# Optimization experiments

Hardware: AMD Instinct MI355X
Metric: run time of the kernel (lower is better)

The kernel has to match this reference:

```python
import jax, jax.numpy as jnp
import numpy as np

B, N, G, H, W = 8, 2000, 100, 320, 320
TRAIN_ROIS = 200
ROI_POS_RATIO = 0.33
NUM_POS = int(TRAIN_ROIS * ROI_POS_RATIO)   # 66 positive slots
NUM_NEG = TRAIN_ROIS - NUM_POS              # 134 negative slots
MASK_H, MASK_W = 28, 28
BBOX_STD = jnp.asarray([0.1, 0.1, 0.2, 0.2], jnp.float32)
EPS = 1e-8


def _rand_boxes(key, shape):
    c = jax.random.uniform(key, shape + (2, 2), dtype=jnp.float32)
    lo, hi = c.min(axis=-2), c.max(axis=-2)
    return jnp.stack([lo[..., 0], lo[..., 1], hi[..., 0], hi[..., 1]], axis=-1)


def setup_inputs() -> dict:
    key = jax.random.key(0)
    k1, k2, k3, k4 = jax.random.split(key, 4)
    proposals = _rand_boxes(k1, (B, N))
    valid = (jnp.arange(G) < G - 20)  # emulate zero-padded GT slots
    prior_boxes = _rand_boxes(k2, (B, G)) * valid[None, :, None]
    prior_class_ids = jax.random.randint(k3, (B, G), 1, 81).astype(jnp.int32) * valid[None, :]
    prior_masks = jax.random.bernoulli(k4, 0.5, (B, H, W, G))
    return {"proposals": proposals, "prior_class_ids": prior_class_ids,
            "prior_boxes": prior_boxes, "prior_masks": prior_masks}


def _iou(a, b):
    # a [N,4], b [G,4], boxes are (y1,x1,y2,x2) -> [N,G]
    y1 = jnp.maximum(a[:, None, 0], b[None, :, 0])
    x1 = jnp.maximum(a[:, None, 1], b[None, :, 1])
    y2 = jnp.minimum(a[:, None, 2], b[None, :, 2])
    x2 = jnp.minimum(a[:, None, 3], b[None, :, 3])
    inter = jnp.maximum(y2 - y1, 0.0) * jnp.maximum(x2 - x1, 0.0)
    area_a = (a[:, 2] - a[:, 0]) * (a[:, 3] - a[:, 1])
    area_b = (b[:, 2] - b[:, 0]) * (b[:, 3] - b[:, 1])
    union = area_a[:, None] + area_b[None, :] - inter
    return inter / jnp.maximum(union, EPS)


def _box_refinement(box, gt):
    h = jnp.maximum(box[:, 2] - box[:, 0], EPS)
    w = jnp.maximum(box[:, 3] - box[:, 1], EPS)
    cy = box[:, 0] + 0.5 * h
    cx = box[:, 1] + 0.5 * w
    gh = jnp.maximum(gt[:, 2] - gt[:, 0], EPS)
    gw = jnp.maximum(gt[:, 3] - gt[:, 1], EPS)
    gcy = gt[:, 0] + 0.5 * gh
    gcx = gt[:, 1] + 0.5 * gw
    return jnp.stack([(gcy - cy) / h, (gcx - cx) / w,
                      jnp.log(gh / h), jnp.log(gw / w)], axis=-1)


def _crop_resize(mask, box):
    # bilinear crop-and-resize of one [H,W] mask to [MASK_H,MASK_W]
    Hm, Wm = mask.shape
    y1, x1, y2, x2 = box[0], box[1], box[2], box[3]
    fy = jnp.arange(MASK_H, dtype=jnp.float32) / (MASK_H - 1)
    fx = jnp.arange(MASK_W, dtype=jnp.float32) / (MASK_W - 1)
    ys = jnp.clip(y1 * (Hm - 1) + fy * (y2 - y1) * (Hm - 1), 0.0, Hm - 1.0)
    xs = jnp.clip(x1 * (Wm - 1) + fx * (x2 - x1) * (Wm - 1), 0.0, Wm - 1.0)
    y0 = jnp.clip(jnp.floor(ys).astype(jnp.int32), 0, Hm - 2)
    x0 = jnp.clip(jnp.floor(xs).astype(jnp.int32), 0, Wm - 2)
    wy, wx = ys - y0, xs - x0
    r0, r1 = mask[y0], mask[y0 + 1]            # [mh, W]
    c00, c01 = r0[:, x0], r0[:, x0 + 1]        # [mh, mw]
    c10, c11 = r1[:, x0], r1[:, x0 + 1]
    top = c00 * (1 - wx)[None, :] + c01 * wx[None, :]
    bot = c10 * (1 - wx)[None, :] + c11 * wx[None, :]
    return top * (1 - wy)[:, None] + bot * wy[:, None]


def _targets_single(proposals, class_ids, gt_boxes, gt_masks):
    valid_prop = jnp.any(jnp.abs(proposals) > 0, axis=1)   # trim zero-padded proposals
    valid_gt = jnp.any(jnp.abs(gt_boxes) > 0, axis=1)      # trim zero-padded GT
    iou = jnp.where(valid_gt[None, :] & valid_prop[:, None],
                    _iou(proposals, gt_boxes), -1.0)       # [N,G]
    roi_iou_max = iou.max(axis=1)

    # positive ROIs: IoU >= 0.5; deterministic hardest-first selection (top-k)
    pos = roi_iou_max >= 0.5
    _, pos_idx = jax.lax.top_k(jnp.where(pos, roi_iou_max, -1.0), NUM_POS)
    pos_count = jnp.minimum(pos.sum(), NUM_POS)
    pos_ok = jnp.arange(NUM_POS) < pos_count

    # negatives: IoU < 0.5, keep positive:negative ratio
    neg = (roi_iou_max < 0.5) & valid_prop
    _, neg_idx = jax.lax.top_k(jnp.where(neg, roi_iou_max, -2.0), NUM_NEG)
    neg_count = (pos_count.astype(jnp.float32) / ROI_POS_RATIO).astype(jnp.int32) - pos_count
    neg_count = jnp.minimum(jnp.minimum(neg_count, neg.sum()), NUM_NEG)
    neg_ok = jnp.arange(NUM_NEG) < neg_count

    pos_rois = jnp.where(pos_ok[:, None], proposals[pos_idx], 0.0)
    gt_assign = jnp.argmax(iou[pos_idx], axis=1)            # [NUM_POS]
    roi_gt = gt_boxes[gt_assign]
    tgt_class = jnp.where(pos_ok, class_ids[gt_assign], 0)
    deltas = jnp.where(pos_ok[:, None], _box_refinement(pos_rois, roi_gt) / BBOX_STD, 0.0)

    # gather assigned GT masks and crop-resize by the positive ROI box (use_mini_mask=False)
    masks_g = jnp.transpose(gt_masks, (2, 0, 1)).astype(jnp.float32)  # [G,H,W]
    crops = jax.vmap(_crop_resize)(masks_g[gt_assign], pos_rois)      # [NUM_POS,mh,mw]
    tgt_mask = jnp.where(pos_ok[:, None, None], jnp.round(crops), 0.0)

    neg_rois = jnp.where(neg_ok[:, None], proposals[neg_idx], 0.0)
    rois = jnp.concatenate([pos_rois, neg_rois], axis=0)
    tgt_class = jnp.concatenate([tgt_class, jnp.zeros((NUM_NEG,), tgt_class.dtype)])
    deltas = jnp.concatenate([deltas, jnp.zeros((NUM_NEG, 4), deltas.dtype)])
    tgt_mask = jnp.concatenate([tgt_mask, jnp.zeros((NUM_NEG, MASK_H, MASK_W), tgt_mask.dtype)])
    return rois, tgt_class, deltas, tgt_mask


def reference(proposals, prior_class_ids, prior_boxes, prior_masks):
    return jax.vmap(_targets_single)(proposals, prior_class_ids, prior_boxes, prior_masks)
```

## Files before the change

kernel.cpp:

```cpp
#include <hip/hip_runtime.h>

#define Bn 8
#define Nn 2000
#define Gn 100
#define Hm 320
#define Wm 320
#define NUM_POS 66
#define NUM_NEG 134
#define TRAIN_ROIS 200
#define MASK_H 28
#define MASK_W 28
#define EPSf 1e-8f

__global__ void k_iou(const float* __restrict__ proposals,
                      const float* __restrict__ gt_boxes,
                      const unsigned int* __restrict__ masks_raw,
                      float* __restrict__ ws_m, int* __restrict__ ws_g,
                      int* __restrict__ flag) {
#pragma clang fp contract(off)
    int b = blockIdx.x;
    int tid = threadIdx.x;
    __shared__ float4 sgt[Gn];
    __shared__ unsigned char svalid[Gn];
    for (int g = tid; g < Gn; g += blockDim.x) {
        const float* q = gt_boxes + (b * Gn + g) * 4;
        float4 bx = make_float4(q[0], q[1], q[2], q[3]);
        sgt[g] = bx;
        svalid[g] = (fabsf(bx.x) > 0.f) || (fabsf(bx.y) > 0.f) ||
                    (fabsf(bx.z) > 0.f) || (fabsf(bx.w) > 0.f);
    }
    if (b == 0 && tid == 0) {
        int f = 0;
        for (int i = 0; i < 64; ++i) {
            unsigned int w = masks_raw[i];
            if (w == 0x3F800000u) { f = 2; break; }
            if (w > 1u) f = 1;
        }
        *flag = f;
    }
    __syncthreads();
    for (int i = tid; i < Nn; i += blockDim.x) {
        const float* pp = proposals + (b * Nn + i) * 4;
        float p0 = pp[0], p1 = pp[1], p2 = pp[2], p3 = pp[3];
        bool vp = (fabsf(p0) > 0.f) || (fabsf(p1) > 0.f) ||
                  (fabsf(p2) > 0.f) || (fabsf(p3) > 0.f);
        float area_a = (p2 - p0) * (p3 - p1);
        float m = -1.0f;
        int best = 0;
        for (int g = 0; g < Gn; ++g) {
            float val = -1.0f;
            if (vp && svalid[g]) {
                float4 q = sgt[g];
                float y1 = fmaxf(p0, q.x);
                float x1 = fmaxf(p1, q.y);
                float y2 = fminf(p2, q.z);
                float x2 = fminf(p3, q.w);
                float inter = fmaxf(y2 - y1, 0.f) * fmaxf(x2 - x1, 0.f);
                float area_b = (q.z - q.x) * (q.w - q.y);
                float uni = area_a + area_b - inter;
                val = inter / fmaxf(uni, EPSf);
            }
            if (val > m) { m = val; best = g; }
        }
        ws_m[b * Nn + i] = m;
        ws_g[b * Nn + i] = best;
    }
}

__global__ __launch_bounds__(1024) void k_select(
        const float* __restrict__ proposals,
        const int* __restrict__ class_ids,
        const float* __restrict__ gt_boxes,
        const float* __restrict__ ws_m,
        const int* __restrict__ ws_g,
        int* __restrict__ posmap,
        float* __restrict__ out) {
#pragma clang fp contract(off)
    int b = blockIdx.x;
    int tid = threadIdx.x;
    __shared__ unsigned long long key[2048];
    __shared__ int cnt_pos, cnt_neg;
    if (tid == 0) { cnt_pos = 0; cnt_neg = 0; }
    __syncthreads();
    for (int i = tid; i < 2048; i += 1024) {
        unsigned long long k;
        if (i < Nn) {
            float m = ws_m[b * Nn + i];
            if (m >= 0.5f) atomicAdd(&cnt_pos, 1);
            else if (m >= 0.0f) atomicAdd(&cnt_neg, 1);
            unsigned int u = __float_as_uint(m);
            u = (u & 0x80000000u) ? ~u : (u | 0x80000000u);
            k = ((unsigned long long)u << 32) | (unsigned int)(~(unsigned int)i);
        } else {
            k = 0ull;
        }
        key[i] = k;
    }
    __syncthreads();
    for (int kk = 2; kk <= 2048; kk <<= 1) {
        for (int j = kk >> 1; j > 0; j >>= 1) {
            for (int i = tid; i < 2048; i += 1024) {
                int ixj = i ^ j;
                if (ixj > i) {
                    bool desc = ((i & kk) == 0);
                    unsigned long long a = key[i], c = key[ixj];
                    if ((a < c) == desc) { key[i] = c; key[ixj] = a; }
                }
            }
            __syncthreads();
        }
    }
    int cp = cnt_pos, cn = cnt_neg;
    int pos_count = min(cp, NUM_POS);
    int nc = (int)((float)pos_count / 0.33f) - pos_count;
    nc = min(nc, cn);
    nc = min(nc, NUM_NEG);

    float* rois = out;
    float* tcls = out + Bn * TRAIN_ROIS * 4;
    float* tdel = tcls + Bn * TRAIN_ROIS;

    if (tid < TRAIN_ROIS) {
        int s = tid;
        float r0 = 0, r1 = 0, r2 = 0, r3 = 0, cls = 0;
        float d0 = 0, d1 = 0, d2 = 0, d3 = 0;
        if (s < NUM_POS) {
            int pi = -1, pg = -1;
            if (s < pos_count) {
                int i = (int)(~(unsigned int)key[s]);
                int g = ws_g[b * Nn + i];
                pi = i; pg = g;
                const float* p = proposals + (b * Nn + i) * 4;
                const float* q = gt_boxes + (b * Gn + g) * 4;
                r0 = p[0]; r1 = p[1]; r2 = p[2]; r3 = p[3];
                cls = (float)class_ids[b * Gn + g];
                float h = fmaxf(p[2] - p[0], EPSf);
                float w = fmaxf(p[3] - p[1], EPSf);
                float cy = p[0] + 0.5f * h, cx = p[1] + 0.5f * w;
                float gh = fmaxf(q[2] - q[0], EPSf);
                float gw = fmaxf(q[3] - q[1], EPSf);
                float gcy = q[0] + 0.5f * gh, gcx = q[1] + 0.5f * gw;
                d0 = ((gcy - cy) / h) / 0.1f;
                d1 = ((gcx - cx) / w) / 0.1f;
                d2 = logf(gh / h) / 0.2f;
                d3 = logf(gw / w) / 0.2f;
            }
            posmap[(b * NUM_POS + s) * 2 + 0] = pi;
            posmap[(b * NUM_POS + s) * 2 + 1] = pg;
        } else {
            int j = s - NUM_POS;
            if (j < nc) {
                int i = (int)(~(unsigned int)key[cp + j]);
                const float* p = proposals + (b * Nn + i) * 4;
                r0 = p[0]; r1 = p[1]; r2 = p[2]; r3 = p[3];
            }
        }
        float* ro = rois + (b * TRAIN_ROIS + s) * 4;
        ro[0] = r0; ro[1] = r1; ro[2] = r2; ro[3] = r3;
        tcls[b * TRAIN_ROIS + s] = cls;
        float* dd = tdel + (b * TRAIN_ROIS + s) * 4;
        dd[0] = d0; dd[1] = d1; dd[2] = d2; dd[3] = d3;
    }
}

__global__ void k_mask(const float* __restrict__ proposals,
                       const void* __restrict__ masks,
                       const int* __restrict__ posmap,
                       const int* __restrict__ flag,
                       float* __restrict__ out_mask) {
#pragma clang fp contract(off)
    int s = blockIdx.x;
    int b = blockIdx.y;
    float* o = out_mask + (long long)(b * TRAIN_ROIS + s) * (MASK_H * MASK_W);
    int pi = -1, pg = 0;
    if (s < NUM_POS) {
        pi = posmap[(b * NUM_POS + s) * 2 + 0];
        pg = posmap[(b * NUM_POS + s) * 2 + 1];
    }
    if (pi < 0) {
        for (int p = threadIdx.x; p < MASK_H * MASK_W; p += blockDim.x) o[p] = 0.f;
        return;
    }
    int f = *flag;
    const float* box = proposals + (b * Nn + pi) * 4;
    float y1 = box[0], x1 = box[1], y2 = box[2], x2 = box[3];
    for (int p = threadIdx.x; p < MASK_H * MASK_W; p += blockDim.x) {
        int py = p / MASK_W, px = p % MASK_W;
        float fy = (float)py / (float)(MASK_H - 1);
        float fx = (float)px / (float)(MASK_W - 1);
        float ys = y1 * (float)(Hm - 1) + (fy * (y2 - y1)) * (float)(Hm - 1);
        ys = fminf(fmaxf(ys, 0.f), (float)(Hm - 1));
        float xs = x1 * (float)(Wm - 1) + (fx * (x2 - x1)) * (float)(Wm - 1);
        xs = fminf(fmaxf(xs, 0.f), (float)(Wm - 1));
        int y0 = min(max((int)floorf(ys), 0), Hm - 2);
        int x0 = min(max((int)floorf(xs), 0), Wm - 2);
        float wy = ys - (float)y0;
        float wx = xs - (float)x0;
        long long i00 = ((long long)(b * Hm + y0) * Wm + x0) * Gn + pg;
        long long i01 = i00 + Gn;
        long long i10 = i00 + (long long)Wm * Gn;
        long long i11 = i10 + Gn;
        float c00, c01, c10, c11;
        if (f == 0) {
            const int* mi = (const int*)masks;
            c00 = (float)mi[i00]; c01 = (float)mi[i01];
            c10 = (float)mi[i10]; c11 = (float)mi[i11];
        } else if (f == 1) {
            const unsigned char* mu = (const unsigned char*)masks;
            c00 = (float)mu[i00]; c01 = (float)mu[i01];
            c10 = (float)mu[i10]; c11 = (float)mu[i11];
        } else {
            const float* mf = (const float*)masks;
            c00 = mf[i00]; c01 = mf[i01];
            c10 = mf[i10]; c11 = mf[i11];
        }
        float top = c00 * (1.f - wx) + c01 * wx;
        float bot = c10 * (1.f - wx) + c11 * wx;
        float v = top * (1.f - wy) + bot * wy;
        o[p] = rintf(v);
    }
}

extern "C" void kernel_launch(void* const* d_in, const int* in_sizes, int n_in,
                              void* d_out, int out_size, void* d_ws, size_t ws_size,
                              hipStream_t stream) {
    const float* proposals = (const float*)d_in[0];
    const int* class_ids = (const int*)d_in[1];
    const float* gt_boxes = (const float*)d_in[2];
    const void* masks = d_in[3];
    float* out = (float*)d_out;

    char* ws = (char*)d_ws;
    float* ws_m = (float*)ws;
    int* ws_g = (int*)(ws + Bn * Nn * 4);
    int* posmap = (int*)(ws + 2 * Bn * Nn * 4);
    int* flag = (int*)(ws + 2 * Bn * Nn * 4 + Bn * NUM_POS * 2 * 4);

    k_iou<<<dim3(Bn), 256, 0, stream>>>(proposals, gt_boxes,
                                        (const unsigned int*)masks,
                                        ws_m, ws_g, flag);
    k_select<<<dim3(Bn), 1024, 0, stream>>>(proposals, class_ids, gt_boxes,
                                            ws_m, ws_g, posmap, out);
    float* out_mask = out + Bn * TRAIN_ROIS * 4 + Bn * TRAIN_ROIS + Bn * TRAIN_ROIS * 4;
    k_mask<<<dim3(TRAIN_ROIS, Bn), 256, 0, stream>>>(proposals, masks, posmap,
                                                     flag, out_mask);
}
```

Baseline: 557.4 us.

## Fuse IoU computation into selection kernel, keep best-GT index in shared memory

Merges the per-proposal IoU/argmax kernel into the sort-and-select kernel. Each of the 1024 threads computes IoU for up to two proposals and writes the sort key and best GT index straight into shared memory. This drops one kernel launch and the global workspace round trip for max IoU and GT index. IoU work now runs on 1024 threads per batch instead of 256, which raises per-block parallelism but still uses only 8 blocks.

```diff
diff --git a/kernel.cpp b/kernel.cpp
--- a/kernel.cpp
+++ b/kernel.cpp
@@ -12,17 +12,24 @@
 #define MASK_W 28
 #define EPSf 1e-8f
 
-__global__ void k_iou(const float* __restrict__ proposals,
-                      const float* __restrict__ gt_boxes,
-                      const unsigned int* __restrict__ masks_raw,
-                      float* __restrict__ ws_m, int* __restrict__ ws_g,
-                      int* __restrict__ flag) {
+__global__ __launch_bounds__(1024) void k_select(
+        const float* __restrict__ proposals,
+        const int* __restrict__ class_ids,
+        const float* __restrict__ gt_boxes,
+        const unsigned int* __restrict__ masks_raw,
+        int* __restrict__ posmap,
+        int* __restrict__ flag,
+        float* __restrict__ out) {
 #pragma clang fp contract(off)
     int b = blockIdx.x;
     int tid = threadIdx.x;
+    __shared__ unsigned long long key[2048];
+    __shared__ unsigned char g_arr[2048];
     __shared__ float4 sgt[Gn];
     __shared__ unsigned char svalid[Gn];
-    for (int g = tid; g < Gn; g += blockDim.x) {
+    __shared__ int cnt_pos, cnt_neg;
+    if (tid == 0) { cnt_pos = 0; cnt_neg = 0; }
+    for (int g = tid; g < Gn; g += 1024) {
         const float* q = gt_boxes + (b * Gn + g) * 4;
         float4 bx = make_float4(q[0], q[1], q[2], q[3]);
         sgt[g] = bx;
@@ -39,60 +46,37 @@
         *flag = f;
     }
     __syncthreads();
-    for (int i = tid; i < Nn; i += blockDim.x) {
-        const float* pp = proposals + (b * Nn + i) * 4;
-        float p0 = pp[0], p1 = pp[1], p2 = pp[2], p3 = pp[3];
-        bool vp = (fabsf(p0) > 0.f) || (fabsf(p1) > 0.f) ||
-                  (fabsf(p2) > 0.f) || (fabsf(p3) > 0.f);
-        float area_a = (p2 - p0) * (p3 - p1);
-        float m = -1.0f;
-        int best = 0;
-        for (int g = 0; g < Gn; ++g) {
-            float val = -1.0f;
-            if (vp && svalid[g]) {
-                float4 q = sgt[g];
-                float y1 = fmaxf(p0, q.x);
-                float x1 = fmaxf(p1, q.y);
-                float y2 = fminf(p2, q.z);
-                float x2 = fminf(p3, q.w);
-                float inter = fmaxf(y2 - y1, 0.f) * fmaxf(x2 - x1, 0.f);
-                float area_b = (q.z - q.x) * (q.w - q.y);
-                float uni = area_a + area_b - inter;
-                val = inter / fmaxf(uni, EPSf);
-            }
-            if (val > m) { m = val; best = g; }
-        }
-        ws_m[b * Nn + i] = m;
-        ws_g[b * Nn + i] = best;
-    }
-}
-
-__global__ __launch_bounds__(1024) void k_select(
-        const float* __restrict__ proposals,
-        const int* __restrict__ class_ids,
-        const float* __restrict__ gt_boxes,
-        const float* __restrict__ ws_m,
-        const int* __restrict__ ws_g,
-        int* __restrict__ posmap,
-        float* __restrict__ out) {
-#pragma clang fp contract(off)
-    int b = blockIdx.x;
-    int tid = threadIdx.x;
-    __shared__ unsigned long long key[2048];
-    __shared__ int cnt_pos, cnt_neg;
-    if (tid == 0) { cnt_pos = 0; cnt_neg = 0; }
-    __syncthreads();
     for (int i = tid; i < 2048; i += 1024) {
-        unsigned long long k;
+        unsigned long long k = 0ull;
         if (i < Nn) {
-            float m = ws_m[b * Nn + i];
+            const float* pp = proposals + (b * Nn + i) * 4;
+            float p0 = pp[0], p1 = pp[1], p2 = pp[2], p3 = pp[3];
+            bool vp = (fabsf(p0) > 0.f) || (fabsf(p1) > 0.f) ||
+                      (fabsf(p2) > 0.f) || (fabsf(p3) > 0.f);
+            float area_a = (p2 - p0) * (p3 - p1);
+            float m = -1.0f;
+            int best = 0;
+            for (int g = 0; g < Gn; ++g) {
+                float val = -1.0f;
+                if (vp && svalid[g]) {
+                    float4 q = sgt[g];
+                    float y1 = fmaxf(p0, q.x);
+                    float x1 = fmaxf(p1, q.y);
+                    float y2 = fminf(p2, q.z);
+                    float x2 = fminf(p3, q.w);
+                    float inter = fmaxf(y2 - y1, 0.f) * fmaxf(x2 - x1, 0.f);
+                    float area_b = (q.z - q.x) * (q.w - q.y);
+                    float uni = area_a + area_b - inter;
+                    val = inter / fmaxf(uni, EPSf);
+                }
+                if (val > m) { m = val; best = g; }
+            }
+            g_arr[i] = (unsigned char)best;
             if (m >= 0.5f) atomicAdd(&cnt_pos, 1);
             else if (m >= 0.0f) atomicAdd(&cnt_neg, 1);
             unsigned int u = __float_as_uint(m);
             u = (u & 0x80000000u) ? ~u : (u | 0x80000000u);
             k = ((unsigned long long)u << 32) | (unsigned int)(~(unsigned int)i);
-        } else {
-            k = 0ull;
         }
         key[i] = k;
     }
@@ -128,7 +112,7 @@
             int pi = -1, pg = -1;
             if (s < pos_count) {
                 int i = (int)(~(unsigned int)key[s]);
-                int g = ws_g[b * Nn + i];
+                int g = (int)g_arr[i];
                 pi = i; pg = g;
                 const float* p = proposals + (b * Nn + i) * 4;
                 const float* q = gt_boxes + (b * Gn + g) * 4;
@@ -231,16 +215,12 @@
     float* out = (float*)d_out;
 
     char* ws = (char*)d_ws;
-    float* ws_m = (float*)ws;
-    int* ws_g = (int*)(ws + Bn * Nn * 4);
-    int* posmap = (int*)(ws + 2 * Bn * Nn * 4);
-    int* flag = (int*)(ws + 2 * Bn * Nn * 4 + Bn * NUM_POS * 2 * 4);
-
-    k_iou<<<dim3(Bn), 256, 0, stream>>>(proposals, gt_boxes,
-                                        (const unsigned int*)masks,
-                                        ws_m, ws_g, flag);
+    int* posmap = (int*)ws;
+    int* flag = (int*)(ws + Bn * NUM_POS * 2 * 4);
+
     k_select<<<dim3(Bn), 1024, 0, stream>>>(proposals, class_ids, gt_boxes,
-                                            ws_m, ws_g, posmap, out);
+                                            (const unsigned int*)masks,
+                                            posmap, flag, out);
     float* out_mask = out + Bn * TRAIN_ROIS * 4 + Bn * TRAIN_ROIS + Bn * TRAIN_ROIS * 4;
     k_mask<<<dim3(TRAIN_ROIS, Bn), 256, 0, stream>>>(proposals, masks, posmap,
                                                      flag, out_mask);
```

Measured after the change: 472.0 us. -15.3%, faster.
